# Optimization experiments

Hardware: AMD Instinct MI355X
Metric: run time of the kernel (lower is better)

Reference implementation:

```python
import jax, jax.numpy as jnp
import numpy as np

N_ATOMS = 4096
BOX = 37.0
CUTOFF = 5.0


def _f_r(r, fe, beta, re, lam):
    # f_e * exp(-beta*(r/r_e - 1)) / (1 + (r/r_e - lamda)^20)
    x = r / re
    return fe * jnp.exp(-beta * (x - 1.0)) / (1.0 + (x - lam) ** 20)


def _phi_r(r, a, b, re, alpha, beta, kappa, lam):
    x = r / re
    l = a * jnp.exp(-alpha * (x - 1.0)) / (1.0 + (x - kappa) ** 20)
    rr = b * jnp.exp(-beta * (x - 1.0)) / (1.0 + (x - lam) ** 20)
    return l - rr


def setup_inputs() -> dict:
    key = jax.random.key(0)
    k1, k2 = jax.random.split(key)
    # coordinates in a box sized for metal-like density so neighbors exist within cutoff
    coords = jax.random.uniform(k1, (N_ATOMS, 3), dtype=jnp.float32) * BOX
    # all 22 EAM parameters positive in [1.0, 2.5] (r_e, rho_s, rho_n, rho_0, eta must be > 0)
    params = 1.0 + 1.5 * jax.random.uniform(k2, (N_ATOMS, 22), dtype=jnp.float32)
    return {"coords": coords, "params": params}


def reference(coords, params):
    N = coords.shape[0]
    # docstring column order: r_e, f_e, rho_e, rho_s, alpha, beta, A, B, kappa, lamda,
    # f_n0..f_n3, f_0..f_3, eta, f_e2, rho_n, rho_0
    r_e, f_e, rho_e, rho_s = params[:, 0], params[:, 1], params[:, 2], params[:, 3]
    alpha, beta = params[:, 4], params[:, 5]
    A, B, kappa, lam = params[:, 6], params[:, 7], params[:, 8], params[:, 9]
    eta, f_e2 = params[:, 18], params[:, 19]
    rho_n, rho_0 = params[:, 20], params[:, 21]

    # ---- full pairwise distances (safe diagonal for differentiable sqrt) ----
    diff = coords[None, :, :] - coords[:, None, :]            # [N, N, 3]
    r2 = jnp.sum(diff * diff, axis=-1)                        # [N, N]
    eye = jnp.eye(N, dtype=bool)
    r_mat = jnp.sqrt(jnp.where(eye, 1.0, r2))                 # [N, N]

    # ---- pair energy over i<j with r <= cutoff (masked, same math as torch filtering) ----
    iu, ju = jnp.triu_indices(N, k=1)                         # P = N(N-1)/2 pairs
    r_pair = r_mat[iu, ju]
    mask = r_pair <= CUTOFF
    r_safe = jnp.where(mask, r_pair, 1.0)                     # nan-safe for masked-out pairs

    fr_i = _f_r(r_safe, f_e[iu], beta[iu], r_e[iu], lam[iu])
    fr_j = _f_r(r_safe, f_e[ju], beta[ju], r_e[ju], lam[ju])
    ph_i = _phi_r(r_safe, A[iu], B[iu], r_e[iu], alpha[iu], beta[iu], kappa[iu], lam[iu])
    ph_j = _phi_r(r_safe, A[ju], B[ju], r_e[ju], alpha[ju], beta[ju], kappa[ju], lam[ju])
    phi_01 = fr_j / fr_i * ph_i + fr_i / fr_j * ph_j
    p_e = 0.5 * jnp.sum(jnp.where(mask, phi_01, 0.0))

    # ---- per-atom density rho_i = sum_{j != i} f_r(r_ij, params_j) (no cutoff, as in source) ----
    fr_mat = _f_r(r_mat, f_e[None, :], beta[None, :], r_e[None, :], lam[None, :])
    rho = jnp.sum(jnp.where(eye, 0.0, fr_mat), axis=1)        # [N]

    # ---- embedding F(rho) with three branches (if/elif/else -> nested where) ----
    xn = rho / rho_n - 1.0
    poly_n = params[:, 10] + params[:, 11] * xn + params[:, 12] * xn ** 2 + params[:, 13] * xn ** 3
    xe = rho / rho_e - 1.0
    poly_0 = params[:, 14] + params[:, 15] * xe + params[:, 16] * xe ** 2 + params[:, 17] * xe ** 3
    t = (rho / rho_s) ** eta
    tail = f_e2 * (1.0 - jnp.log(t)) * t
    F_i = jnp.where(rho < rho_n, poly_n, jnp.where(rho < rho_0, poly_0, tail))

    return p_e + jnp.sum(F_i)
```

## Files before the change

kernel.cpp:

```cpp
#include <hip/hip_runtime.h>
#include <math.h>

#define N_ATOMS 4096
#define CUTOFF2 25.0f
#define NTILE   16
#define NJ      128
#define JT      32
#define LOG2E   1.4426950408889634f
#define LN2     0.6931471805599453f

typedef float v2f __attribute__((ext_vector_type(2)));

__device__ __forceinline__ float pow20f(float t) {
    float t2 = t * t, t4 = t2 * t2, t8 = t4 * t4, t16 = t8 * t8;
    return t16 * t4;
}
__device__ __forceinline__ v2f pow20v(v2f t) {
    v2f t2 = t * t, t4 = t2 * t2, t8 = t4 * t4, t16 = t8 * t8;
    return t16 * t4;
}

__device__ __forceinline__ float block_reduce(float v, float* red) {
    __syncthreads();
    #pragma unroll
    for (int off = 32; off > 0; off >>= 1) v += __shfl_down(v, off, 64);
    if ((threadIdx.x & 63) == 0) red[threadIdx.x >> 6] = v;
    __syncthreads();
    return (red[0] + red[1]) + (red[2] + red[3]);
}

__global__ __launch_bounds__(256) void eam_main(
    const float* __restrict__ coords, const float* __restrict__ params,
    float* __restrict__ rho_part,
    float* __restrict__ e_part)
{
    __shared__ float srho[16 * 16];
    __shared__ float sphi[JT * 16];
    __shared__ float red[4];

    const int tid = threadIdx.x;
    const int bi  = blockIdx.x;
    const int s   = blockIdx.y;
    const int i   = bi * 256 + tid;
    const int jbase = s * JT;

    if (tid < JT) {
        const int j = jbase + tid;
        const float* p = params + 22 * j;
        const float x = coords[3*j], y = coords[3*j+1], z = coords[3*j+2];
        const float rei  = __builtin_amdgcn_rcpf(p[0]);
        const float bl2  = p[5] * LOG2E;
        const float al2  = p[4] * LOG2E;
        const float c0b  = -bl2 * rei;
        const float c1bp = bl2 + __builtin_amdgcn_logf(p[1]);
        const float c0a  = -al2 * rei;
        const float mla  = -p[9];

        float* ph = sphi + 16 * tid;
        ph[0] = x;    ph[1] = y;    ph[2]  = z;     ph[3]  = rei;
        ph[4] = c0b;  ph[5] = c1bp; ph[6]  = mla;   ph[7]  = 0.0f;
        ph[8] = c0a;  ph[9] = al2;  ph[10] = -p[8]; ph[11] = p[6];
        ph[12] = p[7] * __builtin_amdgcn_rcpf(p[1]);

        float* rd = srho + 16 * (tid >> 1) + (tid & 1);
        rd[0] = x;   rd[2]  = y;    rd[4]  = z;   rd[6]  = rei;
        rd[8] = c0b; rd[10] = c1bp; rd[12] = mla;
    }

    const float* pi = params + 22 * i;
    const float xi = coords[3*i], yi = coords[3*i+1], zi = coords[3*i+2];
    const float rei_i  = __builtin_amdgcn_rcpf(pi[0]);
    const float bl2_i  = pi[5] * LOG2E;
    const float al2_i  = pi[4] * LOG2E;
    const float c0b_i  = -bl2_i * rei_i;
    const float c1bp_i = bl2_i + __builtin_amdgcn_logf(pi[1]);
    const float c0a_i  = -al2_i * rei_i;
    const float mla_i  = -pi[9];
    const float mka_i  = -pi[8];
    const float A_i    = pi[6];
    const float Bof_i  = pi[7] * __builtin_amdgcn_rcpf(pi[1]);

    __syncthreads();

    const v2f xi2 = { xi, xi }, yi2 = { yi, yi }, zi2 = { zi, zi };
    v2f rho2 = { 0.0f, 0.0f };
    unsigned int mask = 0;

    const float4* sp4 = (const float4*)srho;
    #pragma unroll 4
    for (int k = 0; k < JT / 2; ++k) {
        const float4 f0 = sp4[k * 4 + 0];
        const float4 f1 = sp4[k * 4 + 1];
        const float4 f2 = sp4[k * 4 + 2];
        const float4 f3 = sp4[k * 4 + 3];
        const v2f x01 = { f0.x, f0.y }, y01 = { f0.z, f0.w };
        const v2f z01 = { f1.x, f1.y }, rei01 = { f1.z, f1.w };
        const v2f c0b01 = { f2.x, f2.y }, c1b01 = { f2.z, f2.w };
        const v2f mla01 = { f3.x, f3.y };

        const v2f dx = x01 - xi2;
        const v2f dy = y01 - yi2;
        const v2f dz = z01 - zi2;
        const v2f r2v = dx * dx + dy * dy + dz * dz;
        const v2f rv = { __builtin_amdgcn_sqrtf(r2v.x), __builtin_amdgcn_sqrtf(r2v.y) };
        const v2f ea = rv * c0b01 + c1b01;
        const v2f ev = { __builtin_amdgcn_exp2f(ea.x), __builtin_amdgcn_exp2f(ea.y) };
        const v2f pa = rv * rei01 + mla01;
        const v2f den = pow20v(pa) + 1.0f;
        const v2f dv = { __builtin_amdgcn_rcpf(den.x), __builtin_amdgcn_rcpf(den.y) };
        rho2 += ev * dv;

        if (r2v.x <= CUTOFF2) mask |= (1u << (2 * k));
        if (r2v.y <= CUTOFF2) mask |= (1u << (2 * k + 1));
    }

    float rho = rho2.x + rho2.y;
    if (i >= jbase && i < jbase + JT) {
        rho -= __builtin_amdgcn_exp2f(c1bp_i)
             * __builtin_amdgcn_rcpf(1.0f + pow20f(mla_i));
    }
    rho_part[(size_t)s * N_ATOMS + i] = rho;

    {
        const int t = i - jbase;
        unsigned int allowed = 0xFFFFFFFFu;
        if (t >= 31)     allowed = 0u;
        else if (t >= 0) allowed = ~((2u << t) - 1u);
        mask &= allowed;
    }

    float e = 0.0f;
    while (mask) {
        const int k = __builtin_ctz(mask);
        mask &= mask - 1;
        const float4 q0 = *(const float4*)&sphi[k * 16];
        const float4 q1 = *(const float4*)&sphi[k * 16 + 4];
        const float4 q2 = *(const float4*)&sphi[k * 16 + 8];
        const float Bof_j = sphi[k * 16 + 12];

        const float dx = q0.x - xi;
        const float dy = q0.y - yi;
        const float dz = q0.z - zi;
        const float r = __builtin_amdgcn_sqrtf(fmaf(dx, dx, fmaf(dy, dy, dz * dz)));

        const float fri = __builtin_amdgcn_exp2f(fmaf(r, c0b_i, c1bp_i))
                        * __builtin_amdgcn_rcpf(1.0f + pow20f(fmaf(r, rei_i, mla_i)));
        const float frj = __builtin_amdgcn_exp2f(fmaf(r, q1.x, q1.y))
                        * __builtin_amdgcn_rcpf(1.0f + pow20f(fmaf(r, q0.w, q1.z)));
        const float ph_i = A_i * __builtin_amdgcn_exp2f(fmaf(r, c0a_i, al2_i))
                               * __builtin_amdgcn_rcpf(1.0f + pow20f(fmaf(r, rei_i, mka_i)))
                         - Bof_i * fri;
        const float ph_j = q2.w * __builtin_amdgcn_exp2f(fmaf(r, q2.x, q2.y))
                                * __builtin_amdgcn_rcpf(1.0f + pow20f(fmaf(r, q0.w, q2.z)))
                         - Bof_j * frj;
        e += 0.5f * fmaf(frj * frj, ph_i, fri * fri * ph_j)
                  * __builtin_amdgcn_rcpf(fri * frj);
    }

    const float eb = block_reduce(e, red);
    if (tid == 0) e_part[bi * NJ + s] = eb;
}

__global__ __launch_bounds__(256) void eam_embed(
    const float* __restrict__ params,
    const float* __restrict__ rho_part, const float* __restrict__ e_part,
    float* __restrict__ tile_sum)
{
    __shared__ float red[4];
    const int tid = threadIdx.x;
    const int bi  = blockIdx.x;
    const int i   = bi * 256 + tid;

    float s0 = 0.0f, s1 = 0.0f, s2 = 0.0f, s3 = 0.0f;
    #pragma unroll 8
    for (int t = 0; t < NJ; t += 4) {
        s0 += rho_part[(size_t)(t + 0) * N_ATOMS + i];
        s1 += rho_part[(size_t)(t + 1) * N_ATOMS + i];
        s2 += rho_part[(size_t)(t + 2) * N_ATOMS + i];
        s3 += rho_part[(size_t)(t + 3) * N_ATOMS + i];
    }
    const float rhoi = (s0 + s1) + (s2 + s3);

    const float* p = params + 22 * i;
    float F;
    if (rhoi < p[20]) {
        const float xn = rhoi / p[20] - 1.0f;
        F = p[10] + xn * (p[11] + xn * (p[12] + xn * p[13]));
    } else if (rhoi < p[21]) {
        const float xe = rhoi / p[2] - 1.0f;
        F = p[14] + xe * (p[15] + xe * (p[16] + xe * p[17]));
    } else {
        const float l2 = __builtin_amdgcn_logf(rhoi / p[3]);
        const float t  = __builtin_amdgcn_exp2f(p[18] * l2);
        const float lt = p[18] * l2 * LN2;
        F = p[19] * (1.0f - lt) * t;
    }

    float acc = F + ((tid < NJ) ? e_part[bi * NJ + tid] : 0.0f);
    const float tot = block_reduce(acc, red);
    if (tid == 0) tile_sum[bi] = tot;
}

__global__ __launch_bounds__(64) void eam_final(
    const float* __restrict__ tile_sum, float* __restrict__ out)
{
    const int tid = threadIdx.x;
    float acc = (tid < NTILE) ? tile_sum[tid] : 0.0f;
    #pragma unroll
    for (int off = 8; off > 0; off >>= 1) acc += __shfl_down(acc, off, 64);
    if (tid == 0) out[0] = acc;
}

extern "C" void kernel_launch(void* const* d_in, const int* in_sizes, int n_in,
                              void* d_out, int out_size, void* d_ws, size_t ws_size,
                              hipStream_t stream) {
    const float* coords = (const float*)d_in[0];
    const float* params = (const float*)d_in[1];
    float* out = (float*)d_out;

    float* rho_part = (float*)d_ws;
    float* e_part   = rho_part + (size_t)NJ * N_ATOMS;
    float* tile_sum = e_part + NTILE * NJ;

    dim3 grid(NTILE, NJ);
    eam_main<<<grid, 256, 0, stream>>>(coords, params, rho_part, e_part);
    eam_embed<<<NTILE, 256, 0, stream>>>(params, rho_part, e_part, tile_sum);
    eam_final<<<1, 64, 0, stream>>>(tile_sum, out);
}
```

Baseline: 25.03 us.

## Prepack per-atom constants and process two i-atoms per thread with smaller j tiles

A new pack kernel precomputes per-atom derived constants into float4-aligned workspace buffers, so the main kernel loads them with vector loads instead of recomputing them per block. Each thread now handles two i-atoms, reusing every shared-memory j entry twice, and the j tile shrinks from 32 to 16 so the grid has 8x256 blocks. In exchange, it adds a fourth kernel launch and doubles the number of rho partials, which the 16-block embed kernel must write and then re-read.

```diff
diff --git a/kernel.cpp b/kernel.cpp
--- a/kernel.cpp
+++ b/kernel.cpp
@@ -3,9 +3,9 @@
 
 #define N_ATOMS 4096
 #define CUTOFF2 25.0f
-#define NTILE   16
-#define NJ      128
-#define JT      32
+#define NI_T    8
+#define NJ      256
+#define JT      16
 #define LOG2E   1.4426950408889634f
 #define LN2     0.6931471805599453f
 
@@ -29,133 +29,167 @@
     return (red[0] + red[1]) + (red[2] + red[3]);
 }
 
+__global__ __launch_bounds__(256) void pack_kernel(
+    const float* __restrict__ coords, const float* __restrict__ params,
+    float* __restrict__ apk, float* __restrict__ rpk)
+{
+    const int a = blockIdx.x * 256 + threadIdx.x;
+    const float* p = params + 22 * a;
+    const float x = coords[3*a], y = coords[3*a+1], z = coords[3*a+2];
+    const float rei  = __builtin_amdgcn_rcpf(p[0]);
+    const float bl2  = p[5] * LOG2E;
+    const float al2  = p[4] * LOG2E;
+    const float c0b  = -bl2 * rei;
+    const float c1bp = bl2 + __builtin_amdgcn_logf(p[1]);
+    const float c0a  = -al2 * rei;
+    const float mla  = -p[9];
+
+    float4* ad = (float4*)(apk + 16 * a);
+    ad[0] = { x, y, z, rei };
+    ad[1] = { c0b, c1bp, mla, 0.0f };
+    ad[2] = { c0a, al2, -p[8], p[6] };
+    ad[3] = { p[7] * __builtin_amdgcn_rcpf(p[1]), 0.0f, 0.0f, 0.0f };
+
+    float* rd = rpk + 16 * (a >> 1) + (a & 1);
+    rd[0] = x;   rd[2]  = y;    rd[4]  = z;   rd[6]  = rei;
+    rd[8] = c0b; rd[10] = c1bp; rd[12] = mla; rd[14] = 0.0f;
+}
+
 __global__ __launch_bounds__(256) void eam_main(
-    const float* __restrict__ coords, const float* __restrict__ params,
+    const float* __restrict__ apk, const float* __restrict__ rpk,
     float* __restrict__ rho_part,
     float* __restrict__ e_part)
 {
-    __shared__ float srho[16 * 16];
-    __shared__ float sphi[JT * 16];
+    __shared__ float4 srho4[JT / 2 * 4];
+    __shared__ float4 sphi4[JT * 4];
     __shared__ float red[4];
 
     const int tid = threadIdx.x;
     const int bi  = blockIdx.x;
     const int s   = blockIdx.y;
-    const int i   = bi * 256 + tid;
+    const int i0  = bi * 512 + tid;
+    const int i1  = i0 + 256;
     const int jbase = s * JT;
 
-    if (tid < JT) {
-        const int j = jbase + tid;
-        const float* p = params + 22 * j;
-        const float x = coords[3*j], y = coords[3*j+1], z = coords[3*j+2];
-        const float rei  = __builtin_amdgcn_rcpf(p[0]);
-        const float bl2  = p[5] * LOG2E;
-        const float al2  = p[4] * LOG2E;
-        const float c0b  = -bl2 * rei;
-        const float c1bp = bl2 + __builtin_amdgcn_logf(p[1]);
-        const float c0a  = -al2 * rei;
-        const float mla  = -p[9];
-
-        float* ph = sphi + 16 * tid;
-        ph[0] = x;    ph[1] = y;    ph[2]  = z;     ph[3]  = rei;
-        ph[4] = c0b;  ph[5] = c1bp; ph[6]  = mla;   ph[7]  = 0.0f;
-        ph[8] = c0a;  ph[9] = al2;  ph[10] = -p[8]; ph[11] = p[6];
-        ph[12] = p[7] * __builtin_amdgcn_rcpf(p[1]);
-
-        float* rd = srho + 16 * (tid >> 1) + (tid & 1);
-        rd[0] = x;   rd[2]  = y;    rd[4]  = z;   rd[6]  = rei;
-        rd[8] = c0b; rd[10] = c1bp; rd[12] = mla;
-    }
-
-    const float* pi = params + 22 * i;
-    const float xi = coords[3*i], yi = coords[3*i+1], zi = coords[3*i+2];
-    const float rei_i  = __builtin_amdgcn_rcpf(pi[0]);
-    const float bl2_i  = pi[5] * LOG2E;
-    const float al2_i  = pi[4] * LOG2E;
-    const float c0b_i  = -bl2_i * rei_i;
-    const float c1bp_i = bl2_i + __builtin_amdgcn_logf(pi[1]);
-    const float c0a_i  = -al2_i * rei_i;
-    const float mla_i  = -pi[9];
-    const float mka_i  = -pi[8];
-    const float A_i    = pi[6];
-    const float Bof_i  = pi[7] * __builtin_amdgcn_rcpf(pi[1]);
+    if (tid < 32)                    srho4[tid]      = ((const float4*)rpk)[s * 32 + tid];
+    else if (tid >= 64 && tid < 128) sphi4[tid - 64] = ((const float4*)apk)[s * 64 + (tid - 64)];
+
+    const float4* apk4 = (const float4*)apk;
+    const float4 a00 = apk4[i0 * 4 + 0], a01 = apk4[i0 * 4 + 1];
+    const float4 a02 = apk4[i0 * 4 + 2], a03 = apk4[i0 * 4 + 3];
+    const float4 a10 = apk4[i1 * 4 + 0], a11 = apk4[i1 * 4 + 1];
+    const float4 a12 = apk4[i1 * 4 + 2], a13 = apk4[i1 * 4 + 3];
 
     __syncthreads();
 
-    const v2f xi2 = { xi, xi }, yi2 = { yi, yi }, zi2 = { zi, zi };
-    v2f rho2 = { 0.0f, 0.0f };
-    unsigned int mask = 0;
-
-    const float4* sp4 = (const float4*)srho;
-    #pragma unroll 4
+    const v2f xi0 = { a00.x, a00.x }, yi0 = { a00.y, a00.y }, zi0 = { a00.z, a00.z };
+    const v2f xi1 = { a10.x, a10.x }, yi1 = { a10.y, a10.y }, zi1 = { a10.z, a10.z };
+
+    v2f rho0v = { 0.0f, 0.0f }, rho1v = { 0.0f, 0.0f };
+    unsigned int m0 = 0, m1 = 0;
+
+    #pragma unroll
     for (int k = 0; k < JT / 2; ++k) {
-        const float4 f0 = sp4[k * 4 + 0];
-        const float4 f1 = sp4[k * 4 + 1];
-        const float4 f2 = sp4[k * 4 + 2];
-        const float4 f3 = sp4[k * 4 + 3];
+        const float4 f0 = srho4[k * 4 + 0];
+        const float4 f1 = srho4[k * 4 + 1];
+        const float4 f2 = srho4[k * 4 + 2];
+        const float4 f3 = srho4[k * 4 + 3];
         const v2f x01 = { f0.x, f0.y }, y01 = { f0.z, f0.w };
         const v2f z01 = { f1.x, f1.y }, rei01 = { f1.z, f1.w };
         const v2f c0b01 = { f2.x, f2.y }, c1b01 = { f2.z, f2.w };
         const v2f mla01 = { f3.x, f3.y };
 
-        const v2f dx = x01 - xi2;
-        const v2f dy = y01 - yi2;
-        const v2f dz = z01 - zi2;
-        const v2f r2v = dx * dx + dy * dy + dz * dz;
-        const v2f rv = { __builtin_amdgcn_sqrtf(r2v.x), __builtin_amdgcn_sqrtf(r2v.y) };
-        const v2f ea = rv * c0b01 + c1b01;
-        const v2f ev = { __builtin_amdgcn_exp2f(ea.x), __builtin_amdgcn_exp2f(ea.y) };
-        const v2f pa = rv * rei01 + mla01;
-        const v2f den = pow20v(pa) + 1.0f;
-        const v2f dv = { __builtin_amdgcn_rcpf(den.x), __builtin_amdgcn_rcpf(den.y) };
-        rho2 += ev * dv;
-
-        if (r2v.x <= CUTOFF2) mask |= (1u << (2 * k));
-        if (r2v.y <= CUTOFF2) mask |= (1u << (2 * k + 1));
-    }
-
-    float rho = rho2.x + rho2.y;
-    if (i >= jbase && i < jbase + JT) {
-        rho -= __builtin_amdgcn_exp2f(c1bp_i)
-             * __builtin_amdgcn_rcpf(1.0f + pow20f(mla_i));
-    }
-    rho_part[(size_t)s * N_ATOMS + i] = rho;
+        {
+            const v2f dx = x01 - xi0, dy = y01 - yi0, dz = z01 - zi0;
+            const v2f r2v = dx * dx + dy * dy + dz * dz;
+            const v2f rv = { __builtin_amdgcn_sqrtf(r2v.x), __builtin_amdgcn_sqrtf(r2v.y) };
+            const v2f ea = rv * c0b01 + c1b01;
+            const v2f ev = { __builtin_amdgcn_exp2f(ea.x), __builtin_amdgcn_exp2f(ea.y) };
+            const v2f pa = rv * rei01 + mla01;
+            const v2f den = pow20v(pa) + 1.0f;
+            const v2f dv = { __builtin_amdgcn_rcpf(den.x), __builtin_amdgcn_rcpf(den.y) };
+            rho0v += ev * dv;
+            if (r2v.x <= CUTOFF2) m0 |= (1u << (2 * k));
+            if (r2v.y <= CUTOFF2) m0 |= (1u << (2 * k + 1));
+        }
+        {
+            const v2f dx = x01 - xi1, dy = y01 - yi1, dz = z01 - zi1;
+            const v2f r2v = dx * dx + dy * dy + dz * dz;
+            const v2f rv = { __builtin_amdgcn_sqrtf(r2v.x), __builtin_amdgcn_sqrtf(r2v.y) };
+            const v2f ea = rv * c0b01 + c1b01;
+            const v2f ev = { __builtin_amdgcn_exp2f(ea.x), __builtin_amdgcn_exp2f(ea.y) };
+            const v2f pa = rv * rei01 + mla01;
+            const v2f den = pow20v(pa) + 1.0f;
+            const v2f dv = { __builtin_amdgcn_rcpf(den.x), __builtin_amdgcn_rcpf(den.y) };
+            rho1v += ev * dv;
+            if (r2v.x <= CUTOFF2) m1 |= (1u << (2 * k));
+            if (r2v.y <= CUTOFF2) m1 |= (1u << (2 * k + 1));
+        }
+    }
+
+    float rho0 = rho0v.x + rho0v.y;
+    float rho1 = rho1v.x + rho1v.y;
+    if (i0 >= jbase && i0 < jbase + JT)
+        rho0 -= __builtin_amdgcn_exp2f(a01.y) * __builtin_amdgcn_rcpf(1.0f + pow20f(a01.z));
+    if (i1 >= jbase && i1 < jbase + JT)
+        rho1 -= __builtin_amdgcn_exp2f(a11.y) * __builtin_amdgcn_rcpf(1.0f + pow20f(a11.z));
+    rho_part[(size_t)s * N_ATOMS + i0] = rho0;
+    rho_part[(size_t)s * N_ATOMS + i1] = rho1;
 
     {
-        const int t = i - jbase;
-        unsigned int allowed = 0xFFFFFFFFu;
-        if (t >= 31)     allowed = 0u;
-        else if (t >= 0) allowed = ~((2u << t) - 1u);
-        mask &= allowed;
+        const int t0 = i0 - jbase;
+        if (t0 >= JT - 1)  m0 = 0u;
+        else if (t0 >= 0)  m0 &= ~((2u << t0) - 1u);
+        const int t1 = i1 - jbase;
+        if (t1 >= JT - 1)  m1 = 0u;
+        else if (t1 >= 0)  m1 &= ~((2u << t1) - 1u);
     }
 
     float e = 0.0f;
-    while (mask) {
-        const int k = __builtin_ctz(mask);
-        mask &= mask - 1;
-        const float4 q0 = *(const float4*)&sphi[k * 16];
-        const float4 q1 = *(const float4*)&sphi[k * 16 + 4];
-        const float4 q2 = *(const float4*)&sphi[k * 16 + 8];
-        const float Bof_j = sphi[k * 16 + 12];
-
-        const float dx = q0.x - xi;
-        const float dy = q0.y - yi;
-        const float dz = q0.z - zi;
+    while (m0) {
+        const int k = __builtin_ctz(m0);
+        m0 &= m0 - 1;
+        const float4 q0 = sphi4[k * 4 + 0];
+        const float4 q1 = sphi4[k * 4 + 1];
+        const float4 q2 = sphi4[k * 4 + 2];
+        const float Bof_j = sphi4[k * 4 + 3].x;
+        const float dx = q0.x - a00.x, dy = q0.y - a00.y, dz = q0.z - a00.z;
         const float r = __builtin_amdgcn_sqrtf(fmaf(dx, dx, fmaf(dy, dy, dz * dz)));
-
-        const float fri = __builtin_amdgcn_exp2f(fmaf(r, c0b_i, c1bp_i))
-                        * __builtin_amdgcn_rcpf(1.0f + pow20f(fmaf(r, rei_i, mla_i)));
+        const float fri = __builtin_amdgcn_exp2f(fmaf(r, a01.x, a01.y))
+                        * __builtin_amdgcn_rcpf(1.0f + pow20f(fmaf(r, a00.w, a01.z)));
         const float frj = __builtin_amdgcn_exp2f(fmaf(r, q1.x, q1.y))
                         * __builtin_amdgcn_rcpf(1.0f + pow20f(fmaf(r, q0.w, q1.z)));
-        const float ph_i = A_i * __builtin_amdgcn_exp2f(fmaf(r, c0a_i, al2_i))
-                               * __builtin_amdgcn_rcpf(1.0f + pow20f(fmaf(r, rei_i, mka_i)))
-                         - Bof_i * fri;
+        const float ph_i = a02.w * __builtin_amdgcn_exp2f(fmaf(r, a02.x, a02.y))
+                                 * __builtin_amdgcn_rcpf(1.0f + pow20f(fmaf(r, a00.w, a02.z)))
+                         - a03.x * fri;
         const float ph_j = q2.w * __builtin_amdgcn_exp2f(fmaf(r, q2.x, q2.y))
                                 * __builtin_amdgcn_rcpf(1.0f + pow20f(fmaf(r, q0.w, q2.z)))
                          - Bof_j * frj;
         e += 0.5f * fmaf(frj * frj, ph_i, fri * fri * ph_j)
                   * __builtin_amdgcn_rcpf(fri * frj);
     }
+    while (m1) {
+        const int k = __builtin_ctz(m1);
+        m1 &= m1 - 1;
+        const float4 q0 = sphi4[k * 4 + 0];
+        const float4 q1 = sphi4[k * 4 + 1];
+        const float4 q2 = sphi4[k * 4 + 2];
+        const float Bof_j = sphi4[k * 4 + 3].x;
+        const float dx = q0.x - a10.x, dy = q0.y - a10.y, dz = q0.z - a10.z;
+        const float r = __builtin_amdgcn_sqrtf(fmaf(dx, dx, fmaf(dy, dy, dz * dz)));
+        const float fri = __builtin_amdgcn_exp2f(fmaf(r, a11.x, a11.y))
+                        * __builtin_amdgcn_rcpf(1.0f + pow20f(fmaf(r, a10.w, a11.z)));
+        const float frj = __builtin_amdgcn_exp2f(fmaf(r, q1.x, q1.y))
+                        * __builtin_amdgcn_rcpf(1.0f + pow20f(fmaf(r, q0.w, q1.z)));
+        const float ph_i = a12.w * __builtin_amdgcn_exp2f(fmaf(r, a12.x, a12.y))
+                                 * __builtin_amdgcn_rcpf(1.0f + pow20f(fmaf(r, a10.w, a12.z)))
+                         - a13.x * fri;
+        const float ph_j = q2.w * __builtin_amdgcn_exp2f(fmaf(r, q2.x, q2.y))
+                                * __builtin_amdgcn_rcpf(1.0f + pow20f(fmaf(r, q0.w, q2.z)))
+                         - Bof_j * frj;
+        e += 0.5f * fmaf(frj * frj, ph_i, fri * fri * ph_j)
+                  * __builtin_amdgcn_rcpf(fri * frj);
+    }
 
     const float eb = block_reduce(e, red);
     if (tid == 0) e_part[bi * NJ + s] = eb;
@@ -168,8 +202,8 @@
 {
     __shared__ float red[4];
     const int tid = threadIdx.x;
-    const int bi  = blockIdx.x;
-    const int i   = bi * 256 + tid;
+    const int b   = blockIdx.x;
+    const int i   = b * 256 + tid;
 
     float s0 = 0.0f, s1 = 0.0f, s2 = 0.0f, s3 = 0.0f;
     #pragma unroll 8
@@ -196,16 +230,16 @@
         F = p[19] * (1.0f - lt) * t;
     }
 
-    float acc = F + ((tid < NJ) ? e_part[bi * NJ + tid] : 0.0f);
+    float acc = F + ((tid < 128) ? e_part[b * 128 + tid] : 0.0f);
     const float tot = block_reduce(acc, red);
-    if (tid == 0) tile_sum[bi] = tot;
+    if (tid == 0) tile_sum[b] = tot;
 }
 
 __global__ __launch_bounds__(64) void eam_final(
     const float* __restrict__ tile_sum, float* __restrict__ out)
 {
     const int tid = threadIdx.x;
-    float acc = (tid < NTILE) ? tile_sum[tid] : 0.0f;
+    float acc = (tid < 16) ? tile_sum[tid] : 0.0f;
     #pragma unroll
     for (int off = 8; off > 0; off >>= 1) acc += __shfl_down(acc, off, 64);
     if (tid == 0) out[0] = acc;
@@ -218,12 +252,15 @@
     const float* params = (const float*)d_in[1];
     float* out = (float*)d_out;
 
-    float* rho_part = (float*)d_ws;
+    float* apk      = (float*)d_ws;
+    float* rpk      = apk + (size_t)N_ATOMS * 16;
+    float* rho_part = rpk + (size_t)(N_ATOMS / 2) * 16;
     float* e_part   = rho_part + (size_t)NJ * N_ATOMS;
-    float* tile_sum = e_part + NTILE * NJ;
-
-    dim3 grid(NTILE, NJ);
-    eam_main<<<grid, 256, 0, stream>>>(coords, params, rho_part, e_part);
-    eam_embed<<<NTILE, 256, 0, stream>>>(params, rho_part, e_part, tile_sum);
+    float* tile_sum = e_part + NI_T * NJ;
+
+    pack_kernel<<<N_ATOMS / 256, 256, 0, stream>>>(coords, params, apk, rpk);
+    dim3 grid(NI_T, NJ);
+    eam_main<<<grid, 256, 0, stream>>>(apk, rpk, rho_part, e_part);
+    eam_embed<<<16, 256, 0, stream>>>(params, rho_part, e_part, tile_sum);
     eam_final<<<1, 64, 0, stream>>>(tile_sum, out);
 }
```

Result: slower. 44.74 us (+78.7%).

## Precompute packed per-atom params and broadcast j-atoms via readlane

Applied to the files above, without the earlier changes.

Adds a pack kernel that computes the derived per-atom coefficients once into a 16-float record, so the main kernel no longer recomputes them in every block. The main kernel doubles the j-tile to 64, halves the number of y-blocks, and reads j-atom data from registers with readlane instead of LDS float4 loads. It drops the packed-pair v2f math in favour of scalar math with two accumulators. This costs an extra kernel launch and a workspace round-trip, and the larger tile lengthens the per-block loop and divergent pair loop.

```diff
diff --git a/kernel.cpp b/kernel.cpp
--- a/kernel.cpp
+++ b/kernel.cpp
@@ -4,20 +4,18 @@
 #define N_ATOMS 4096
 #define CUTOFF2 25.0f
 #define NTILE   16
-#define NJ      128
-#define JT      32
+#define NJ      64
+#define JT      64
 #define LOG2E   1.4426950408889634f
 #define LN2     0.6931471805599453f
-
-typedef float v2f __attribute__((ext_vector_type(2)));
 
 __device__ __forceinline__ float pow20f(float t) {
     float t2 = t * t, t4 = t2 * t2, t8 = t4 * t4, t16 = t8 * t8;
     return t16 * t4;
 }
-__device__ __forceinline__ v2f pow20v(v2f t) {
-    v2f t2 = t * t, t4 = t2 * t2, t8 = t4 * t4, t16 = t8 * t8;
-    return t16 * t4;
+
+__device__ __forceinline__ float rl(float v, int k) {
+    return __int_as_float(__builtin_amdgcn_readlane(__float_as_int(v), k));
 }
 
 __device__ __forceinline__ float block_reduce(float v, float* red) {
@@ -29,132 +27,115 @@
     return (red[0] + red[1]) + (red[2] + red[3]);
 }
 
+__global__ __launch_bounds__(256) void pack_kernel(
+    const float* __restrict__ coords, const float* __restrict__ params,
+    float* __restrict__ apk)
+{
+    const int a = blockIdx.x * 256 + threadIdx.x;
+    const float* p = params + 22 * a;
+    const float rei  = __builtin_amdgcn_rcpf(p[0]);
+    const float bl2  = p[5] * LOG2E;
+    const float al2  = p[4] * LOG2E;
+    float4* ad = (float4*)(apk + 16 * a);
+    ad[0] = { coords[3*a], coords[3*a+1], coords[3*a+2], rei };
+    ad[1] = { -bl2 * rei, bl2 + __builtin_amdgcn_logf(p[1]), -p[9], 0.0f };
+    ad[2] = { -al2 * rei, al2, -p[8], p[6] };
+    ad[3] = { p[7] * __builtin_amdgcn_rcpf(p[1]), 0.0f, 0.0f, 0.0f };
+}
+
 __global__ __launch_bounds__(256) void eam_main(
-    const float* __restrict__ coords, const float* __restrict__ params,
+    const float* __restrict__ apk,
     float* __restrict__ rho_part,
     float* __restrict__ e_part)
 {
-    __shared__ float srho[16 * 16];
-    __shared__ float sphi[JT * 16];
+    __shared__ float4 sphi4[JT * 4];
     __shared__ float red[4];
 
-    const int tid = threadIdx.x;
-    const int bi  = blockIdx.x;
-    const int s   = blockIdx.y;
-    const int i   = bi * 256 + tid;
+    const int tid  = threadIdx.x;
+    const int bi   = blockIdx.x;
+    const int s    = blockIdx.y;
+    const int i    = bi * 256 + tid;
+    const int lane = tid & 63;
     const int jbase = s * JT;
 
-    if (tid < JT) {
-        const int j = jbase + tid;
-        const float* p = params + 22 * j;
-        const float x = coords[3*j], y = coords[3*j+1], z = coords[3*j+2];
-        const float rei  = __builtin_amdgcn_rcpf(p[0]);
-        const float bl2  = p[5] * LOG2E;
-        const float al2  = p[4] * LOG2E;
-        const float c0b  = -bl2 * rei;
-        const float c1bp = bl2 + __builtin_amdgcn_logf(p[1]);
-        const float c0a  = -al2 * rei;
-        const float mla  = -p[9];
-
-        float* ph = sphi + 16 * tid;
-        ph[0] = x;    ph[1] = y;    ph[2]  = z;     ph[3]  = rei;
-        ph[4] = c0b;  ph[5] = c1bp; ph[6]  = mla;   ph[7]  = 0.0f;
-        ph[8] = c0a;  ph[9] = al2;  ph[10] = -p[8]; ph[11] = p[6];
-        ph[12] = p[7] * __builtin_amdgcn_rcpf(p[1]);
-
-        float* rd = srho + 16 * (tid >> 1) + (tid & 1);
-        rd[0] = x;   rd[2]  = y;    rd[4]  = z;   rd[6]  = rei;
-        rd[8] = c0b; rd[10] = c1bp; rd[12] = mla;
-    }
-
-    const float* pi = params + 22 * i;
-    const float xi = coords[3*i], yi = coords[3*i+1], zi = coords[3*i+2];
-    const float rei_i  = __builtin_amdgcn_rcpf(pi[0]);
-    const float bl2_i  = pi[5] * LOG2E;
-    const float al2_i  = pi[4] * LOG2E;
-    const float c0b_i  = -bl2_i * rei_i;
-    const float c1bp_i = bl2_i + __builtin_amdgcn_logf(pi[1]);
-    const float c0a_i  = -al2_i * rei_i;
-    const float mla_i  = -pi[9];
-    const float mka_i  = -pi[8];
-    const float A_i    = pi[6];
-    const float Bof_i  = pi[7] * __builtin_amdgcn_rcpf(pi[1]);
+    const float4* apk4 = (const float4*)apk;
+    sphi4[tid] = apk4[jbase * 4 + tid];
+
+    const float4 j0 = apk4[(jbase + lane) * 4 + 0];
+    const float4 j1 = apk4[(jbase + lane) * 4 + 1];
+
+    const float4 a0 = apk4[i * 4 + 0];
+    const float4 a1 = apk4[i * 4 + 1];
+    const float4 a2 = apk4[i * 4 + 2];
+    const float4 a3 = apk4[i * 4 + 3];
 
     __syncthreads();
 
-    const v2f xi2 = { xi, xi }, yi2 = { yi, yi }, zi2 = { zi, zi };
-    v2f rho2 = { 0.0f, 0.0f };
-    unsigned int mask = 0;
-
-    const float4* sp4 = (const float4*)srho;
-    #pragma unroll 4
-    for (int k = 0; k < JT / 2; ++k) {
-        const float4 f0 = sp4[k * 4 + 0];
-        const float4 f1 = sp4[k * 4 + 1];
-        const float4 f2 = sp4[k * 4 + 2];
-        const float4 f3 = sp4[k * 4 + 3];
-        const v2f x01 = { f0.x, f0.y }, y01 = { f0.z, f0.w };
-        const v2f z01 = { f1.x, f1.y }, rei01 = { f1.z, f1.w };
-        const v2f c0b01 = { f2.x, f2.y }, c1b01 = { f2.z, f2.w };
-        const v2f mla01 = { f3.x, f3.y };
-
-        const v2f dx = x01 - xi2;
-        const v2f dy = y01 - yi2;
-        const v2f dz = z01 - zi2;
-        const v2f r2v = dx * dx + dy * dy + dz * dz;
-        const v2f rv = { __builtin_amdgcn_sqrtf(r2v.x), __builtin_amdgcn_sqrtf(r2v.y) };
-        const v2f ea = rv * c0b01 + c1b01;
-        const v2f ev = { __builtin_amdgcn_exp2f(ea.x), __builtin_amdgcn_exp2f(ea.y) };
-        const v2f pa = rv * rei01 + mla01;
-        const v2f den = pow20v(pa) + 1.0f;
-        const v2f dv = { __builtin_amdgcn_rcpf(den.x), __builtin_amdgcn_rcpf(den.y) };
-        rho2 += ev * dv;
-
-        if (r2v.x <= CUTOFF2) mask |= (1u << (2 * k));
-        if (r2v.y <= CUTOFF2) mask |= (1u << (2 * k + 1));
-    }
-
-    float rho = rho2.x + rho2.y;
-    if (i >= jbase && i < jbase + JT) {
-        rho -= __builtin_amdgcn_exp2f(c1bp_i)
-             * __builtin_amdgcn_rcpf(1.0f + pow20f(mla_i));
+    float rhoA = 0.0f, rhoB = 0.0f;
+    unsigned int m_lo = 0u, m_hi = 0u;
+
+    #pragma unroll 8
+    for (int k = 0; k < JT; ++k) {
+        const float xj  = rl(j0.x, k), yj = rl(j0.y, k), zj = rl(j0.z, k);
+        const float rej = rl(j0.w, k);
+        const float c0b = rl(j1.x, k), c1b = rl(j1.y, k), mla = rl(j1.z, k);
+
+        const float dx = xj - a0.x;
+        const float dy = yj - a0.y;
+        const float dz = zj - a0.z;
+        const float r2 = fmaf(dx, dx, fmaf(dy, dy, dz * dz));
+        const float r  = __builtin_amdgcn_sqrtf(r2);
+        const float ev = __builtin_amdgcn_exp2f(fmaf(r, c0b, c1b));
+        const float dv = __builtin_amdgcn_rcpf(1.0f + pow20f(fmaf(r, rej, mla)));
+        if (k & 1) rhoB = fmaf(ev, dv, rhoB); else rhoA = fmaf(ev, dv, rhoA);
+
+        const bool hit = (r2 <= CUTOFF2);
+        if (k < 32) m_lo |= hit ? (1u << k) : 0u;
+        else        m_hi |= hit ? (1u << (k - 32)) : 0u;
+    }
+
+    float rho = rhoA + rhoB;
+    const int t = i - jbase;
+    if (t >= 0 && t < JT) {
+        rho -= __builtin_amdgcn_exp2f(a1.y)
+             * __builtin_amdgcn_rcpf(1.0f + pow20f(a1.z));
     }
     rho_part[(size_t)s * N_ATOMS + i] = rho;
 
-    {
-        const int t = i - jbase;
-        unsigned int allowed = 0xFFFFFFFFu;
-        if (t >= 31)     allowed = 0u;
-        else if (t >= 0) allowed = ~((2u << t) - 1u);
-        mask &= allowed;
-    }
-
+    if (t >= 63)      { m_lo = 0u; m_hi = 0u; }
+    else if (t >= 32) { m_lo = 0u; m_hi &= ~((2u << (t - 32)) - 1u); }
+    else if (t >= 0)  { m_lo &= ~((2u << t) - 1u); }
+
+    const float* sphi = (const float*)sphi4;
     float e = 0.0f;
-    while (mask) {
-        const int k = __builtin_ctz(mask);
-        mask &= mask - 1;
-        const float4 q0 = *(const float4*)&sphi[k * 16];
-        const float4 q1 = *(const float4*)&sphi[k * 16 + 4];
-        const float4 q2 = *(const float4*)&sphi[k * 16 + 8];
-        const float Bof_j = sphi[k * 16 + 12];
-
-        const float dx = q0.x - xi;
-        const float dy = q0.y - yi;
-        const float dz = q0.z - zi;
-        const float r = __builtin_amdgcn_sqrtf(fmaf(dx, dx, fmaf(dy, dy, dz * dz)));
-
-        const float fri = __builtin_amdgcn_exp2f(fmaf(r, c0b_i, c1bp_i))
-                        * __builtin_amdgcn_rcpf(1.0f + pow20f(fmaf(r, rei_i, mla_i)));
-        const float frj = __builtin_amdgcn_exp2f(fmaf(r, q1.x, q1.y))
-                        * __builtin_amdgcn_rcpf(1.0f + pow20f(fmaf(r, q0.w, q1.z)));
-        const float ph_i = A_i * __builtin_amdgcn_exp2f(fmaf(r, c0a_i, al2_i))
-                               * __builtin_amdgcn_rcpf(1.0f + pow20f(fmaf(r, rei_i, mka_i)))
-                         - Bof_i * fri;
-        const float ph_j = q2.w * __builtin_amdgcn_exp2f(fmaf(r, q2.x, q2.y))
-                                * __builtin_amdgcn_rcpf(1.0f + pow20f(fmaf(r, q0.w, q2.z)))
-                         - Bof_j * frj;
-        e += 0.5f * fmaf(frj * frj, ph_i, fri * fri * ph_j)
-                  * __builtin_amdgcn_rcpf(fri * frj);
+    #pragma unroll 1
+    for (int half = 0; half < 2; ++half) {
+        unsigned int m = half ? m_hi : m_lo;
+        const int kofs = half ? 32 : 0;
+        while (m) {
+            const int k = __builtin_ctz(m) + kofs;
+            m &= m - 1;
+            const float4 q0 = *(const float4*)&sphi[k * 16];
+            const float4 q1 = *(const float4*)&sphi[k * 16 + 4];
+            const float4 q2 = *(const float4*)&sphi[k * 16 + 8];
+            const float Bof_j = sphi[k * 16 + 12];
+
+            const float dx = q0.x - a0.x, dy = q0.y - a0.y, dz = q0.z - a0.z;
+            const float r = __builtin_amdgcn_sqrtf(fmaf(dx, dx, fmaf(dy, dy, dz * dz)));
+
+            const float fri = __builtin_amdgcn_exp2f(fmaf(r, a1.x, a1.y))
+                            * __builtin_amdgcn_rcpf(1.0f + pow20f(fmaf(r, a0.w, a1.z)));
+            const float frj = __builtin_amdgcn_exp2f(fmaf(r, q1.x, q1.y))
+                            * __builtin_amdgcn_rcpf(1.0f + pow20f(fmaf(r, q0.w, q1.z)));
+            const float ph_i = a2.w * __builtin_amdgcn_exp2f(fmaf(r, a2.x, a2.y))
+                                    * __builtin_amdgcn_rcpf(1.0f + pow20f(fmaf(r, a0.w, a2.z)))
+                             - a3.x * fri;
+            const float ph_j = q2.w * __builtin_amdgcn_exp2f(fmaf(r, q2.x, q2.y))
+                                    * __builtin_amdgcn_rcpf(1.0f + pow20f(fmaf(r, q0.w, q2.z)))
+                             - Bof_j * frj;
+            e += 0.5f * fmaf(frj * frj, ph_i, fri * fri * ph_j)
+                      * __builtin_amdgcn_rcpf(fri * frj);
+        }
     }
 
     const float eb = block_reduce(e, red);
@@ -168,11 +149,11 @@
 {
     __shared__ float red[4];
     const int tid = threadIdx.x;
-    const int bi  = blockIdx.x;
-    const int i   = bi * 256 + tid;
+    const int b   = blockIdx.x;
+    const int i   = b * 256 + tid;
 
     float s0 = 0.0f, s1 = 0.0f, s2 = 0.0f, s3 = 0.0f;
-    #pragma unroll 8
+    #pragma unroll 4
     for (int t = 0; t < NJ; t += 4) {
         s0 += rho_part[(size_t)(t + 0) * N_ATOMS + i];
         s1 += rho_part[(size_t)(t + 1) * N_ATOMS + i];
@@ -196,9 +177,9 @@
         F = p[19] * (1.0f - lt) * t;
     }
 
-    float acc = F + ((tid < NJ) ? e_part[bi * NJ + tid] : 0.0f);
+    float acc = F + ((tid < NJ) ? e_part[b * NJ + tid] : 0.0f);
     const float tot = block_reduce(acc, red);
-    if (tid == 0) tile_sum[bi] = tot;
+    if (tid == 0) tile_sum[b] = tot;
 }
 
 __global__ __launch_bounds__(64) void eam_final(
@@ -218,12 +199,14 @@
     const float* params = (const float*)d_in[1];
     float* out = (float*)d_out;
 
-    float* rho_part = (float*)d_ws;
+    float* apk      = (float*)d_ws;
+    float* rho_part = apk + (size_t)N_ATOMS * 16;
     float* e_part   = rho_part + (size_t)NJ * N_ATOMS;
     float* tile_sum = e_part + NTILE * NJ;
 
+    pack_kernel<<<N_ATOMS / 256, 256, 0, stream>>>(coords, params, apk);
     dim3 grid(NTILE, NJ);
-    eam_main<<<grid, 256, 0, stream>>>(coords, params, rho_part, e_part);
-    eam_embed<<<NTILE, 256, 0, stream>>>(params, rho_part, e_part, tile_sum);
+    eam_main<<<grid, 256, 0, stream>>>(apk, rho_part, e_part);
+    eam_embed<<<16, 256, 0, stream>>>(params, rho_part, e_part, tile_sum);
     eam_final<<<1, 64, 0, stream>>>(tile_sum, out);
 }
```

Measured after the change: 38.52 us. +53.9%, slower.
